# Performance work log

Measured on AMD Instinct MI355X. Metric: run time of the kernel, lower is better.

The kernel has to match this reference:

```python
import jax, jax.numpy as jnp
import numpy as np

B, L1, L2, H = 8, 384, 384, 128


def _lin(k, out_f, in_f, scale=0.05):
    kw, kb = jax.random.split(k)
    return (jax.random.normal(kw, (out_f, in_f), jnp.float32) * scale,
            jax.random.normal(kb, (out_f,), jnp.float32) * scale)


def setup_inputs() -> dict:
    key = jax.random.key(0)
    ks = jax.random.split(key, 10)
    Wq_w, Wq_b = _lin(ks[2], H, H)
    Wup_w, Wup_b = _lin(ks[3], H, H)
    Wvp_w, Wvp_b = _lin(ks[4], H, H)
    V_w, V_b = _lin(ks[5], 1, H)
    Wg_w, Wg_b = _lin(ks[6], 2 * H, 2 * H)
    W_ih, b_ih = _lin(ks[7], 4 * H, 2 * H)
    W_hh, b_hh = _lin(ks[8], 4 * H, H)
    return {
        "x": jax.random.normal(ks[0], (B, L1, H), jnp.float32),
        "x_mask": jnp.zeros((B, L1), dtype=bool),
        "y": jax.random.normal(ks[1], (B, L2, H), jnp.float32),
        "y_mask": jnp.zeros((B, L2), dtype=bool),
        "Wq_w": Wq_w, "Wq_b": Wq_b,
        "Wup_w": Wup_w, "Wup_b": Wup_b,
        "Wvp_w": Wvp_w, "Wvp_b": Wvp_b,
        "V_w": V_w, "V_b": V_b,
        "Wg_w": Wg_w, "Wg_b": Wg_b,
        "W_ih": W_ih, "W_hh": W_hh, "b_ih": b_ih, "b_hh": b_hh,
    }


def reference(x, x_mask, y, y_mask, Wq_w, Wq_b, Wup_w, Wup_b, Wvp_w, Wvp_b,
              V_w, V_b, Wg_w, Wg_b, W_ih, W_hh, b_ih, b_hh):
    b, l1, h = x.shape
    # projections (torch Linear: x @ W.T + b)
    x_proj = x @ Wup_w.T + Wup_b                      # [B, L1, H]
    y_proj = y @ Wq_w.T + Wq_b                        # [B, L2, H]
    # source feeds a constant zero hidden state into W_vp -> just its bias
    hidden_proj = jnp.zeros((h,), x.dtype) @ Wvp_w.T + Wvp_b  # [H]
    # additive attention scores: V . tanh(xp + yp + hp)
    sum_batch = jnp.tanh(x_proj[:, :, None, :] + y_proj[:, None, :, :] + hidden_proj)  # [B,L1,L2,H]
    s = jnp.einsum('btjh,h->btj', sum_batch, V_w[0]) + V_b[0]  # [B, L1, L2]
    # sum_mask = (1 - x_mask) outer (1 - y_mask)
    xm = 1.0 - x_mask.astype(s.dtype)
    ym = 1.0 - y_mask.astype(s.dtype)
    s = s * (xm[:, :, None] * ym[:, None, :])
    s = jnp.where(y_mask[:, None, :], -jnp.inf, s)
    alpha = jax.nn.softmax(s, axis=-1)                # [B, L1, L2]
    ct = jnp.einsum('btj,bjh->bth', alpha, y)         # [B, L1, H]
    merge = jnp.concatenate([x, ct], axis=2)          # [B, L1, 2H]
    gt = jax.nn.sigmoid(merge @ Wg_w.T + Wg_b)
    lstm_in = gt * merge                              # [B, L1, 2H]
    # single-layer unidirectional LSTM (torch gate order: i, f, g, o)
    gates_x = lstm_in @ W_ih.T + b_ih                 # [B, L1, 4H]

    def step(carry, gx):
        h_t, c_t = carry
        g = gx + h_t @ W_hh.T + b_hh
        i, f, gg, o = jnp.split(g, 4, axis=-1)
        c_n = jax.nn.sigmoid(f) * c_t + jax.nn.sigmoid(i) * jnp.tanh(gg)
        h_n = jax.nn.sigmoid(o) * jnp.tanh(c_n)
        return (h_n, c_n), h_n

    init = (jnp.zeros((b, h), x.dtype), jnp.zeros((b, h), x.dtype))
    _, hs = jax.lax.scan(step, init, jnp.swapaxes(gates_x, 0, 1))  # [L1, B, H]
    return jnp.swapaxes(hs, 0, 1)                     # [B, L1, H]
```

## Files before the change

kernel.cpp:

```cpp
#include <hip/hip_runtime.h>
#include <hip/hip_bf16.h>
#include <math.h>

typedef __attribute__((ext_vector_type(4))) float  float4v;
typedef __attribute__((ext_vector_type(2))) float  float2v;
typedef __attribute__((ext_vector_type(8))) short  short8;

#define B_ 8
#define L_ 384
#define H_ 128

__device__ __forceinline__ float bflo(unsigned int u){ unsigned int t = u << 16; float f; __builtin_memcpy(&f,&t,4); return f; }
__device__ __forceinline__ unsigned short f2bf(float f){
  unsigned int t; __builtin_memcpy(&t,&f,4);
  return (unsigned short)((t + 0x7fffu + ((t>>16)&1u)) >> 16);
}
__device__ __forceinline__ float fsig(float x){ return __fdividef(1.f, 1.f + __expf(-x)); }

__device__ __forceinline__ void barrier_lds(){
  asm volatile("s_waitcnt lgkmcnt(0)\n\ts_barrier" ::: "memory");
}

template<int K>
__device__ __forceinline__ void mfma_rowgemm_body(
    unsigned short* in_s,
    const float* __restrict__ inA, const float* __restrict__ inB,
    const float* __restrict__ W, const float* __restrict__ bias,
    const float* __restrict__ bias2, float* __restrict__ out,
    int Ntotal, int act, int row0, int ob)
{
  constexpr int KP = K + 2;
  const int tid  = threadIdx.x;
  const int w    = tid >> 6;
  const int l    = tid & 63;
  const int c    = l & 15;
  const int quad = l >> 4;

  #pragma unroll
  for (int it = 0; it < K/32; ++it) {
    int idx = it*256 + tid;
    int r = idx / (K/4);
    int k = (idx % (K/4)) * 4;
    float4v f;
    if (inB != nullptr && k >= 128)
      f = *(const float4v*)(inB + (size_t)(row0+r)*128 + (k-128));
    else if (inB != nullptr)
      f = *(const float4v*)(inA + (size_t)(row0+r)*128 + k);
    else
      f = *(const float4v*)(inA + (size_t)(row0+r)*K + k);
    unsigned int p0 = (unsigned int)f2bf(f.x) | ((unsigned int)f2bf(f.y) << 16);
    unsigned int p1 = (unsigned int)f2bf(f.z) | ((unsigned int)f2bf(f.w) << 16);
    *(unsigned int*)&in_s[r*KP + k]     = p0;
    *(unsigned int*)&in_s[r*KP + k + 2] = p1;
  }

  const int n = ob + w*16 + c;
  short8 bfr[K/32];
  #pragma unroll
  for (int kt = 0; kt < K/32; ++kt) {
    const float* src = W + (size_t)n*K + kt*32 + quad*8;
    float4v f0 = *(const float4v*)(src);
    float4v f1 = *(const float4v*)(src + 4);
    short8 v;
    v[0]=(short)f2bf(f0[0]); v[1]=(short)f2bf(f0[1]); v[2]=(short)f2bf(f0[2]); v[3]=(short)f2bf(f0[3]);
    v[4]=(short)f2bf(f1[0]); v[5]=(short)f2bf(f1[1]); v[6]=(short)f2bf(f1[2]); v[7]=(short)f2bf(f1[3]);
    bfr[kt] = v;
  }
  __syncthreads();

  const float4v z4 = {0.f,0.f,0.f,0.f};
  float4v acc0 = z4, acc1 = z4;
  #pragma unroll
  for (int kt = 0; kt < K/32; ++kt) {
    short8 a0 = *(const short8*)&in_s[(c     )*KP + kt*32 + quad*8];
    short8 a1 = *(const short8*)&in_s[(16 + c)*KP + kt*32 + quad*8];
    acc0 = __builtin_amdgcn_mfma_f32_16x16x32_bf16(a0, bfr[kt], acc0, 0,0,0);
    acc1 = __builtin_amdgcn_mfma_f32_16x16x32_bf16(a1, bfr[kt], acc1, 0,0,0);
  }

  float bv = bias[n] + (bias2 ? bias2[n] : 0.f);
  #pragma unroll
  for (int mt = 0; mt < 2; ++mt) {
    float4v A = mt ? acc1 : acc0;
    #pragma unroll
    for (int r = 0; r < 4; ++r) {
      int m = mt*16 + quad*4 + r;
      float val = A[r] + bv;
      if (act == 2) {
        float mg = bflo((unsigned int)in_s[m*KP + n]);
        val = fsig(val) * mg;
      }
      if (act == 3)
        out[(size_t)(row0+m)*Ntotal + (n & 127)*4 + (n >> 7)] = val;
      else
        out[(size_t)(row0+m)*Ntotal + n] = val;
    }
  }
}

template<int K>
__global__ __launch_bounds__(256) void mfma_rowgemm_kernel(
    const float* __restrict__ inA, const float* __restrict__ inB,
    const float* __restrict__ W, const float* __restrict__ bias,
    const float* __restrict__ bias2, float* __restrict__ out,
    int Ntotal, int act)
{
  __shared__ __align__(16) unsigned short in_s[32*(K+2)];
  mfma_rowgemm_body<K>(in_s, inA, inB, W, bias, bias2, out,
                       Ntotal, act, blockIdx.x*32, blockIdx.y*64);
}

__global__ __launch_bounds__(256) void proj_mfma_kernel(
    const float* __restrict__ x, const float* __restrict__ y,
    const float* __restrict__ Wup_w, const float* __restrict__ Wup_b,
    const float* __restrict__ Wq_w, const float* __restrict__ Wq_b,
    const float* __restrict__ Wvp_b,
    float* __restrict__ xp, float* __restrict__ yp)
{
  __shared__ __align__(16) unsigned short in_s[32*130];
  int bx = blockIdx.x;
  if (bx < 192)
    mfma_rowgemm_body<128>(in_s, x, nullptr, Wup_w, Wup_b, nullptr,
                           xp, 128, 0, (bx>>1)*32, (bx&1)*64);
  else {
    bx -= 192;
    mfma_rowgemm_body<128>(in_s, y, nullptr, Wq_w, Wq_b, Wvp_b,
                           yp, 128, 0, (bx>>1)*32, (bx&1)*64);
  }
}

__global__ __launch_bounds__(256) void attn_kernel(
    const float* __restrict__ xp, const float* __restrict__ yp,
    const float* __restrict__ y, const unsigned char* __restrict__ xmask,
    const unsigned char* __restrict__ ymask, const float* __restrict__ Vw,
    const float* __restrict__ Vb,
    float* __restrict__ ctp0, float* __restrict__ ctp1,
    float* __restrict__ ml)
{
  __shared__ __align__(16) float xp_s[8][128];
  __shared__ __align__(16) float v2_s[128];
  __shared__ __align__(16) float yp_s[32][132];
  __shared__ __align__(16) float yc_s[32][132];
  __shared__ float xm_s[8];
  __shared__ float ym_s[32];
  __shared__ float sv_s;
  const int tid = threadIdx.x;
  const int b   = blockIdx.y;
  const int t0  = blockIdx.x * 8;
  const int jh  = blockIdx.z;
  const float C2 = 2.8853900817779268f;
  {
    int r = tid >> 5, k4 = (tid & 31) * 4;
    float4v f = *(const float4v*)(xp + ((size_t)(b*L_ + t0 + r))*H_ + k4);
    float4v g; g[0]=f[0]*C2; g[1]=f[1]*C2; g[2]=f[2]*C2; g[3]=f[3]*C2;
    *(float4v*)&xp_s[r][k4] = g;
    if (tid < 32) {
      float4v v = *(const float4v*)(Vw + tid*4);
      float4v v2; v2[0]=2.f*v[0]; v2[1]=2.f*v[1]; v2[2]=2.f*v[2]; v2[3]=2.f*v[3];
      *(float4v*)&v2_s[tid*4] = v2;
    }
    if (tid < 8) xm_s[tid] = xmask[b*L_ + t0 + tid] ? 0.f : 1.f;
  }
  __syncthreads();
  if (tid < 32) {
    float4v v = *(const float4v*)&v2_s[tid*4];
    float sm = (v[0]+v[1]) + (v[2]+v[3]);
    #pragma unroll
    for (int off = 16; off >= 1; off >>= 1) sm += __shfl_xor(sm, off);
    if (tid == 0) sv_s = 0.5f*sm + Vb[0];
  }

  float4v rp[4], ry[4];
  unsigned char ymb = 0;
  {
    #pragma unroll
    for (int it = 0; it < 4; ++it) {
      int idx = it*256 + tid; int r = idx >> 5; int k4 = (idx & 31) * 4;
      size_t base = ((size_t)(b*L_ + jh*192 + r))*H_ + k4;
      rp[it] = *(const float4v*)(yp + base);
      ry[it] = *(const float4v*)(y + base);
    }
    if (tid < 32) ymb = ymask[b*L_ + jh*192 + tid];
  }

  const int t = tid >> 5, u = tid & 31;
  float mrun = -__builtin_inff(), lrun = 0.f;
  float a0=0.f, a1=0.f, a2=0.f, a3=0.f;
  float svc = 0.f, xmv = 0.f;

  for (int c = 0; c < 6; ++c) {
    __syncthreads();
    #pragma unroll
    for (int it = 0; it < 4; ++it) {
      int idx = it*256 + tid; int r = idx >> 5; int k4 = (idx & 31) * 4;
      float4v sp; sp[0]=rp[it][0]*C2; sp[1]=rp[it][1]*C2; sp[2]=rp[it][2]*C2; sp[3]=rp[it][3]*C2;
      *(float4v*)&yp_s[r][k4] = sp;
      *(float4v*)&yc_s[r][k4] = ry[it];
    }
    if (tid < 32) ym_s[tid] = ymb ? 0.f : 1.f;
    __syncthreads();
    if (c == 0) { svc = sv_s; xmv = xm_s[t]; }
    if (c < 5) {
      #pragma unroll
      for (int it = 0; it < 4; ++it) {
        int idx = it*256 + tid; int r = idx >> 5; int k4 = (idx & 31) * 4;
        size_t base = ((size_t)(b*L_ + jh*192 + (c+1)*32 + r))*H_ + k4;
        rp[it] = *(const float4v*)(yp + base);
        ry[it] = *(const float4v*)(y + base);
      }
      if (tid < 32) ymb = ymask[b*L_ + jh*192 + (c+1)*32 + tid];
    }

    float sA = 0.f, sB = 0.f;
    {
      const float* yr = yp_s[u];
      const float* xr = xp_s[t];
      #pragma unroll 4
      for (int k = 0; k < 128; k += 4) {
        float4v yv = *(const float4v*)&yr[k];
        float4v xv = *(const float4v*)&xr[k];
        float4v vv = *(const float4v*)&v2_s[k];
        float e0 = __builtin_amdgcn_exp2f(xv[0] + yv[0]);
        sA -= vv[0] * __builtin_amdgcn_rcpf(e0 + 1.f);
        float e1 = __builtin_amdgcn_exp2f(xv[1] + yv[1]);
        sB -= vv[1] * __builtin_amdgcn_rcpf(e1 + 1.f);
        float e2 = __builtin_amdgcn_exp2f(xv[2] + yv[2]);
        sA -= vv[2] * __builtin_amdgcn_rcpf(e2 + 1.f);
        float e3 = __builtin_amdgcn_exp2f(xv[3] + yv[3]);
        sB -= vv[3] * __builtin_amdgcn_rcpf(e3 + 1.f);
      }
    }
    float ymv = ym_s[u];
    float s = (svc + sA + sB) * xmv * ymv;
    if (ymv == 0.f) s = -__builtin_inff();
    float mc = s;
    #pragma unroll
    for (int off = 16; off >= 1; off >>= 1) mc = fmaxf(mc, __shfl_xor(mc, off));
    float mnew = fmaxf(mrun, mc);
    float p  = __expf(s - mnew);
    float sc = __expf(mrun - mnew);
    float ps = p;
    #pragma unroll
    for (int off = 16; off >= 1; off >>= 1) ps += __shfl_xor(ps, off);
    lrun = lrun * sc + ps;
    mrun = mnew;
    a0 *= sc; a1 *= sc; a2 *= sc; a3 *= sc;
    #pragma unroll 8
    for (int j = 0; j < 32; ++j) {
      float pv = __shfl(p, j, 32);
      float4v yv = *(const float4v*)&yc_s[j][u*4];
      a0 += pv*yv[0]; a1 += pv*yv[1]; a2 += pv*yv[2]; a3 += pv*yv[3];
    }
  }
  const int row = b*L_ + t0 + t;
  float* ctp = jh ? ctp1 : ctp0;
  float4v ov; ov[0]=a0; ov[1]=a1; ov[2]=a2; ov[3]=a3;
  *(float4v*)(ctp + (size_t)row*H_ + u*4) = ov;
  if (u == 0) {
    ml[(jh*2+0)*3072 + row] = mrun;
    ml[(jh*2+1)*3072 + row] = lrun;
  }
}

__global__ __launch_bounds__(256) void attn_merge_kernel(
    const float* __restrict__ ctp0, const float* __restrict__ ctp1,
    const float* __restrict__ ml, float* __restrict__ ct)
{
  const int tid = threadIdx.x;
  const int row = blockIdx.x*8 + (tid >> 5);
  const int c4  = (tid & 31) * 4;
  float m0 = ml[row],        l0 = ml[3072 + row];
  float m1 = ml[2*3072+row], l1 = ml[3*3072 + row];
  float m  = fmaxf(m0, m1);
  float e0 = __expf(m0 - m), e1 = __expf(m1 - m);
  float inv = __fdividef(1.f, l0*e0 + l1*e1);
  float4v v0 = *(const float4v*)(ctp0 + (size_t)row*H_ + c4);
  float4v v1 = *(const float4v*)(ctp1 + (size_t)row*H_ + c4);
  float4v r;
  r[0] = (v0[0]*e0 + v1[0]*e1)*inv;
  r[1] = (v0[1]*e0 + v1[1]*e1)*inv;
  r[2] = (v0[2]*e0 + v1[2]*e1)*inv;
  r[3] = (v0[3]*e0 + v1[3]*e1)*inv;
  *(float4v*)(ct + (size_t)row*H_ + c4) = r;
}

__global__ __launch_bounds__(512) void lstm_kernel(
    const float* __restrict__ gx, const float* __restrict__ Whh,
    float* __restrict__ out)
{
  __shared__ __align__(16) unsigned short h_s[2][128];
  const int tid  = threadIdx.x;
  const int b    = blockIdx.x;
  const int w    = tid >> 6;
  const int l    = tid & 63;
  const int col  = l & 15;
  const int quad = l >> 4;

  short8 bf[4][4];
  #pragma unroll
  for (int nt = 0; nt < 4; ++nt) {
    const int n = nt*128 + w*16 + col;
    #pragma unroll
    for (int kt = 0; kt < 4; ++kt) {
      const int k0 = kt*32 + quad*8;
      const float* src = Whh + (size_t)n*H_ + k0;
      float4v f0 = *(const float4v*)(src);
      float4v f1 = *(const float4v*)(src + 4);
      short8 v;
      v[0]=(short)f2bf(f0[0]); v[1]=(short)f2bf(f0[1]); v[2]=(short)f2bf(f0[2]); v[3]=(short)f2bf(f0[3]);
      v[4]=(short)f2bf(f1[0]); v[5]=(short)f2bf(f1[1]); v[6]=(short)f2bf(f1[2]); v[7]=(short)f2bf(f1[3]);
      bf[nt][kt] = v;
    }
  }

  if (tid < 128) { h_s[0][tid] = 0; h_s[1][tid] = 0; }
  float cst = 0.f;
  const int goff = w*16 + col;
  const float* gbase = gx + (size_t)b*L_*512 + goff*4;
  float* outp = out + (size_t)b*L_*H_ + goff;
  float4v gbuf[4];
  #pragma unroll
  for (int s = 0; s < 4; ++s)
    gbuf[s] = *(const float4v*)(gbase + (size_t)s*512);
  const float4v z4 = {0.f,0.f,0.f,0.f};
  const float NL2E = -1.4426950408889634f;
  const float P2L2E = 2.8853900817779268f;
  __syncthreads();

  for (int t4 = 0; t4 < L_; t4 += 4) {
    #pragma unroll
    for (int s = 0; s < 4; ++s) {
      const int tstep = t4 + s;
      const unsigned short* hb = h_s[s & 1];
      short8 a[4];
      #pragma unroll
      for (int kt=0;kt<4;++kt) a[kt] = *(const short8*)&hb[kt*32 + quad*8];
      float4v c0 = z4, c1 = z4, c2 = z4, c3 = z4;
      #pragma unroll
      for (int kt=0;kt<4;++kt) {
        c0 = __builtin_amdgcn_mfma_f32_16x16x32_bf16(a[kt], bf[0][kt], c0, 0,0,0);
        c1 = __builtin_amdgcn_mfma_f32_16x16x32_bf16(a[kt], bf[1][kt], c1, 0,0,0);
        c2 = __builtin_amdgcn_mfma_f32_16x16x32_bf16(a[kt], bf[2][kt], c2, 0,0,0);
        c3 = __builtin_amdgcn_mfma_f32_16x16x32_bf16(a[kt], bf[3][kt], c3, 0,0,0);
      }
      float g0 = c0[0] + gbuf[s][0];
      float g1 = c1[0] + gbuf[s][1];
      float g2 = c2[0] + gbuf[s][2];
      float g3 = c3[0] + gbuf[s][3];
      if (tstep + 4 < L_)
        gbuf[s] = *(const float4v*)(gbase + (size_t)(tstep+4)*512);
      if (quad == 0) {
        float ig = __builtin_amdgcn_rcpf(1.f + __builtin_amdgcn_exp2f(NL2E*g0));
        float fg = __builtin_amdgcn_rcpf(1.f + __builtin_amdgcn_exp2f(NL2E*g1));
        float gg = 1.f - 2.f*__builtin_amdgcn_rcpf(__builtin_amdgcn_exp2f(P2L2E*g2) + 1.f);
        float og = __builtin_amdgcn_rcpf(1.f + __builtin_amdgcn_exp2f(NL2E*g3));
        cst = fg*cst + ig*gg;
        float hn = og * (1.f - 2.f*__builtin_amdgcn_rcpf(__builtin_amdgcn_exp2f(P2L2E*cst) + 1.f));
        outp[(size_t)tstep*H_] = hn;
        h_s[(s+1)&1][goff] = f2bf(hn);
      }
      barrier_lds();
    }
  }
}

extern "C" void kernel_launch(void* const* d_in, const int* in_sizes, int n_in,
                              void* d_out, int out_size, void* d_ws, size_t ws_size,
                              hipStream_t stream)
{
  (void)in_sizes; (void)n_in; (void)out_size; (void)ws_size;
  const float* x     = (const float*)d_in[0];
  const unsigned char* xm = (const unsigned char*)d_in[1];
  const float* y     = (const float*)d_in[2];
  const unsigned char* ym = (const unsigned char*)d_in[3];
  const float* Wq_w  = (const float*)d_in[4];
  const float* Wq_b  = (const float*)d_in[5];
  const float* Wup_w = (const float*)d_in[6];
  const float* Wup_b = (const float*)d_in[7];
  const float* Wvp_b = (const float*)d_in[9];
  const float* V_w   = (const float*)d_in[10];
  const float* V_b   = (const float*)d_in[11];
  const float* Wg_w  = (const float*)d_in[12];
  const float* Wg_b  = (const float*)d_in[13];
  const float* W_ih  = (const float*)d_in[14];
  const float* W_hh  = (const float*)d_in[15];
  const float* b_ih  = (const float*)d_in[16];
  const float* b_hh  = (const float*)d_in[17];
  float* out = (float*)d_out;

  float* wsf    = (float*)d_ws;
  float* xp_ws  = wsf;
  float* yp_ws  = xp_ws + 393216;
  float* ct_ws  = yp_ws + 393216;
  float* li_ws  = ct_ws + 393216;
  float* gx_ws  = li_ws + 786432;
  float* ct2_ws = gx_ws + 1572864;
  float* ml_ws  = ct2_ws + 393216;

  proj_mfma_kernel<<<dim3(384),256,0,stream>>>(x, y, Wup_w, Wup_b, Wq_w, Wq_b, Wvp_b, xp_ws, yp_ws);
  attn_kernel<<<dim3(48,8,2),256,0,stream>>>(xp_ws, yp_ws, y, xm, ym, V_w, V_b, ct_ws, ct2_ws, ml_ws);
  attn_merge_kernel<<<dim3(384),256,0,stream>>>(ct_ws, ct2_ws, ml_ws, ct_ws);
  mfma_rowgemm_kernel<256><<<dim3(96,4),256,0,stream>>>(x, ct_ws, Wg_w, Wg_b, nullptr, li_ws, 256, 2);
  mfma_rowgemm_kernel<256><<<dim3(96,8),256,0,stream>>>(li_ws, nullptr, W_ih, b_ih, b_hh, gx_ws, 512, 3);
  lstm_kernel<<<dim3(8),512,0,stream>>>(gx_ws, W_hh, out);
}
```

Baseline: 345.4 us.

## Fuse attention merge, gate GEMM and input-gate GEMM into one kernel

Replaces the attention-merge kernel and the two row-GEMM launches (gate sigmoid and W_ih projection) with a single 48-block kernel. Each block merges the split-softmax partials on load, computes the gated LSTM input in LDS as bf16, then runs the W_ih GEMM straight from LDS. This removes two launches and the global round-trips for ct and lstm_in. In exchange there are only 48 blocks, so occupancy is low on a large GPU, and each block re-converts the full weight matrices.

```diff
diff --git a/kernel.cpp b/kernel.cpp
--- a/kernel.cpp
+++ b/kernel.cpp
@@ -24,10 +24,10 @@
 template<int K>
 __device__ __forceinline__ void mfma_rowgemm_body(
     unsigned short* in_s,
-    const float* __restrict__ inA, const float* __restrict__ inB,
+    const float* __restrict__ inA,
     const float* __restrict__ W, const float* __restrict__ bias,
     const float* __restrict__ bias2, float* __restrict__ out,
-    int Ntotal, int act, int row0, int ob)
+    int Ntotal, int row0, int ob)
 {
   constexpr int KP = K + 2;
   const int tid  = threadIdx.x;
@@ -41,13 +41,7 @@
     int idx = it*256 + tid;
     int r = idx / (K/4);
     int k = (idx % (K/4)) * 4;
-    float4v f;
-    if (inB != nullptr && k >= 128)
-      f = *(const float4v*)(inB + (size_t)(row0+r)*128 + (k-128));
-    else if (inB != nullptr)
-      f = *(const float4v*)(inA + (size_t)(row0+r)*128 + k);
-    else
-      f = *(const float4v*)(inA + (size_t)(row0+r)*K + k);
+    float4v f = *(const float4v*)(inA + (size_t)(row0+r)*K + k);
     unsigned int p0 = (unsigned int)f2bf(f.x) | ((unsigned int)f2bf(f.y) << 16);
     unsigned int p1 = (unsigned int)f2bf(f.z) | ((unsigned int)f2bf(f.w) << 16);
     *(unsigned int*)&in_s[r*KP + k]     = p0;
@@ -85,29 +79,9 @@
     #pragma unroll
     for (int r = 0; r < 4; ++r) {
       int m = mt*16 + quad*4 + r;
-      float val = A[r] + bv;
-      if (act == 2) {
-        float mg = bflo((unsigned int)in_s[m*KP + n]);
-        val = fsig(val) * mg;
-      }
-      if (act == 3)
-        out[(size_t)(row0+m)*Ntotal + (n & 127)*4 + (n >> 7)] = val;
-      else
-        out[(size_t)(row0+m)*Ntotal + n] = val;
-    }
-  }
-}
-
-template<int K>
-__global__ __launch_bounds__(256) void mfma_rowgemm_kernel(
-    const float* __restrict__ inA, const float* __restrict__ inB,
-    const float* __restrict__ W, const float* __restrict__ bias,
-    const float* __restrict__ bias2, float* __restrict__ out,
-    int Ntotal, int act)
-{
-  __shared__ __align__(16) unsigned short in_s[32*(K+2)];
-  mfma_rowgemm_body<K>(in_s, inA, inB, W, bias, bias2, out,
-                       Ntotal, act, blockIdx.x*32, blockIdx.y*64);
+      out[(size_t)(row0+m)*Ntotal + n] = A[r] + bv;
+    }
+  }
 }
 
 __global__ __launch_bounds__(256) void proj_mfma_kernel(
@@ -120,12 +94,12 @@
   __shared__ __align__(16) unsigned short in_s[32*130];
   int bx = blockIdx.x;
   if (bx < 192)
-    mfma_rowgemm_body<128>(in_s, x, nullptr, Wup_w, Wup_b, nullptr,
-                           xp, 128, 0, (bx>>1)*32, (bx&1)*64);
+    mfma_rowgemm_body<128>(in_s, x, Wup_w, Wup_b, nullptr,
+                           xp, 128, (bx>>1)*32, (bx&1)*64);
   else {
     bx -= 192;
-    mfma_rowgemm_body<128>(in_s, y, nullptr, Wq_w, Wq_b, Wvp_b,
-                           yp, 128, 0, (bx>>1)*32, (bx&1)*64);
+    mfma_rowgemm_body<128>(in_s, y, Wq_w, Wq_b, Wvp_b,
+                           yp, 128, (bx>>1)*32, (bx&1)*64);
   }
 }
 
@@ -262,26 +236,152 @@
   }
 }
 
-__global__ __launch_bounds__(256) void attn_merge_kernel(
+__global__ __launch_bounds__(512) void fused_gate_kernel(
+    const float* __restrict__ x,
     const float* __restrict__ ctp0, const float* __restrict__ ctp1,
-    const float* __restrict__ ml, float* __restrict__ ct)
+    const float* __restrict__ ml,
+    const float* __restrict__ Wg_w, const float* __restrict__ Wg_b,
+    const float* __restrict__ W_ih, const float* __restrict__ b_ih,
+    const float* __restrict__ b_hh, float* __restrict__ gx)
 {
-  const int tid = threadIdx.x;
-  const int row = blockIdx.x*8 + (tid >> 5);
-  const int c4  = (tid & 31) * 4;
-  float m0 = ml[row],        l0 = ml[3072 + row];
-  float m1 = ml[2*3072+row], l1 = ml[3*3072 + row];
-  float m  = fmaxf(m0, m1);
-  float e0 = __expf(m0 - m), e1 = __expf(m1 - m);
-  float inv = __fdividef(1.f, l0*e0 + l1*e1);
-  float4v v0 = *(const float4v*)(ctp0 + (size_t)row*H_ + c4);
-  float4v v1 = *(const float4v*)(ctp1 + (size_t)row*H_ + c4);
-  float4v r;
-  r[0] = (v0[0]*e0 + v1[0]*e1)*inv;
-  r[1] = (v0[1]*e0 + v1[1]*e1)*inv;
-  r[2] = (v0[2]*e0 + v1[2]*e1)*inv;
-  r[3] = (v0[3]*e0 + v1[3]*e1)*inv;
-  *(float4v*)(ct + (size_t)row*H_ + c4) = r;
+  constexpr int KP = 258;
+  constexpr int LP = 264;
+  __shared__ __align__(16) unsigned short in_s[64*KP];
+  __shared__ __align__(16) unsigned short li_s[64*LP];
+  const int tid  = threadIdx.x;
+  const int w    = tid >> 6;
+  const int l    = tid & 63;
+  const int c    = l & 15;
+  const int quad = l >> 4;
+  const int row0 = blockIdx.x * 64;
+  const float4v z4 = {0.f,0.f,0.f,0.f};
+
+  #pragma unroll
+  for (int it = 0; it < 8; ++it) {
+    int idx = it*512 + tid;
+    int r = idx >> 6;
+    int k = (idx & 63) * 4;
+    int row = row0 + r;
+    float4v f;
+    if (k < 128) {
+      f = *(const float4v*)(x + (size_t)row*128 + k);
+    } else {
+      float m0 = ml[row],        l0 = ml[3072 + row];
+      float m1 = ml[2*3072+row], l1 = ml[3*3072 + row];
+      float mm = fmaxf(m0, m1);
+      float e0 = __expf(m0 - mm), e1 = __expf(m1 - mm);
+      float inv = __fdividef(1.f, l0*e0 + l1*e1);
+      float4v v0 = *(const float4v*)(ctp0 + (size_t)row*128 + (k-128));
+      float4v v1 = *(const float4v*)(ctp1 + (size_t)row*128 + (k-128));
+      f[0] = (v0[0]*e0 + v1[0]*e1)*inv;
+      f[1] = (v0[1]*e0 + v1[1]*e1)*inv;
+      f[2] = (v0[2]*e0 + v1[2]*e1)*inv;
+      f[3] = (v0[3]*e0 + v1[3]*e1)*inv;
+    }
+    unsigned int p0 = (unsigned int)f2bf(f[0]) | ((unsigned int)f2bf(f[1]) << 16);
+    unsigned int p1 = (unsigned int)f2bf(f[2]) | ((unsigned int)f2bf(f[3]) << 16);
+    *(unsigned int*)&in_s[r*KP + k]     = p0;
+    *(unsigned int*)&in_s[r*KP + k + 2] = p1;
+  }
+  __syncthreads();
+
+  {
+    short8 bfr[2][8];
+    #pragma unroll
+    for (int i = 0; i < 2; ++i) {
+      int n = (w + i*8)*16 + c;
+      #pragma unroll
+      for (int kt = 0; kt < 8; ++kt) {
+        const float* src = Wg_w + (size_t)n*256 + kt*32 + quad*8;
+        float4v f0 = *(const float4v*)(src);
+        float4v f1 = *(const float4v*)(src + 4);
+        short8 v;
+        v[0]=(short)f2bf(f0[0]); v[1]=(short)f2bf(f0[1]); v[2]=(short)f2bf(f0[2]); v[3]=(short)f2bf(f0[3]);
+        v[4]=(short)f2bf(f1[0]); v[5]=(short)f2bf(f1[1]); v[6]=(short)f2bf(f1[2]); v[7]=(short)f2bf(f1[3]);
+        bfr[i][kt] = v;
+      }
+    }
+    float4v acc[2][4];
+    #pragma unroll
+    for (int i=0;i<2;++i)
+      #pragma unroll
+      for (int mt=0;mt<4;++mt) acc[i][mt] = z4;
+    #pragma unroll
+    for (int kt = 0; kt < 8; ++kt) {
+      short8 a[4];
+      #pragma unroll
+      for (int mt = 0; mt < 4; ++mt)
+        a[mt] = *(const short8*)&in_s[(mt*16 + c)*KP + kt*32 + quad*8];
+      #pragma unroll
+      for (int i = 0; i < 2; ++i)
+        #pragma unroll
+        for (int mt = 0; mt < 4; ++mt)
+          acc[i][mt] = __builtin_amdgcn_mfma_f32_16x16x32_bf16(a[mt], bfr[i][kt], acc[i][mt], 0,0,0);
+    }
+    #pragma unroll
+    for (int i = 0; i < 2; ++i) {
+      int n = (w + i*8)*16 + c;
+      float bv = Wg_b[n];
+      #pragma unroll
+      for (int mt = 0; mt < 4; ++mt)
+        #pragma unroll
+        for (int r = 0; r < 4; ++r) {
+          int m = mt*16 + quad*4 + r;
+          float val = acc[i][mt][r] + bv;
+          float mg = bflo((unsigned int)in_s[m*KP + n]);
+          li_s[m*LP + n] = f2bf(fsig(val) * mg);
+        }
+    }
+  }
+  __syncthreads();
+
+  #pragma unroll
+  for (int p = 0; p < 2; ++p) {
+    short8 bfr[2][8];
+    #pragma unroll
+    for (int i = 0; i < 2; ++i) {
+      int n = (w + i*8 + p*16)*16 + c;
+      #pragma unroll
+      for (int kt = 0; kt < 8; ++kt) {
+        const float* src = W_ih + (size_t)n*256 + kt*32 + quad*8;
+        float4v f0 = *(const float4v*)(src);
+        float4v f1 = *(const float4v*)(src + 4);
+        short8 v;
+        v[0]=(short)f2bf(f0[0]); v[1]=(short)f2bf(f0[1]); v[2]=(short)f2bf(f0[2]); v[3]=(short)f2bf(f0[3]);
+        v[4]=(short)f2bf(f1[0]); v[5]=(short)f2bf(f1[1]); v[6]=(short)f2bf(f1[2]); v[7]=(short)f2bf(f1[3]);
+        bfr[i][kt] = v;
+      }
+    }
+    float4v acc[2][4];
+    #pragma unroll
+    for (int i=0;i<2;++i)
+      #pragma unroll
+      for (int mt=0;mt<4;++mt) acc[i][mt] = z4;
+    #pragma unroll
+    for (int kt = 0; kt < 8; ++kt) {
+      short8 a[4];
+      #pragma unroll
+      for (int mt = 0; mt < 4; ++mt)
+        a[mt] = *(const short8*)&li_s[(mt*16 + c)*LP + kt*32 + quad*8];
+      #pragma unroll
+      for (int i = 0; i < 2; ++i)
+        #pragma unroll
+        for (int mt = 0; mt < 4; ++mt)
+          acc[i][mt] = __builtin_amdgcn_mfma_f32_16x16x32_bf16(a[mt], bfr[i][kt], acc[i][mt], 0,0,0);
+    }
+    #pragma unroll
+    for (int i = 0; i < 2; ++i) {
+      int n = (w + i*8 + p*16)*16 + c;
+      float bv = b_ih[n] + b_hh[n];
+      #pragma unroll
+      for (int mt = 0; mt < 4; ++mt)
+        #pragma unroll
+        for (int r = 0; r < 4; ++r) {
+          int m = mt*16 + quad*4 + r;
+          gx[(size_t)(row0+m)*512 + (n & 127)*4 + (n >> 7)] = acc[i][mt][r] + bv;
+        }
+    }
+  }
 }
 
 __global__ __launch_bounds__(512) void lstm_kernel(
@@ -391,16 +491,14 @@
   float* wsf    = (float*)d_ws;
   float* xp_ws  = wsf;
   float* yp_ws  = xp_ws + 393216;
-  float* ct_ws  = yp_ws + 393216;
-  float* li_ws  = ct_ws + 393216;
-  float* gx_ws  = li_ws + 786432;
-  float* ct2_ws = gx_ws + 1572864;
-  float* ml_ws  = ct2_ws + 393216;
+  float* ctp0_ws= yp_ws + 393216;
+  float* ctp1_ws= ctp0_ws + 393216;
+  float* gx_ws  = ctp1_ws + 393216;
+  float* ml_ws  = gx_ws + 1572864;
 
   proj_mfma_kernel<<<dim3(384),256,0,stream>>>(x, y, Wup_w, Wup_b, Wq_w, Wq_b, Wvp_b, xp_ws, yp_ws);
-  attn_kernel<<<dim3(48,8,2),256,0,stream>>>(xp_ws, yp_ws, y, xm, ym, V_w, V_b, ct_ws, ct2_ws, ml_ws);
-  attn_merge_kernel<<<dim3(384),256,0,stream>>>(ct_ws, ct2_ws, ml_ws, ct_ws);
-  mfma_rowgemm_kernel<256><<<dim3(96,4),256,0,stream>>>(x, ct_ws, Wg_w, Wg_b, nullptr, li_ws, 256, 2);
-  mfma_rowgemm_kernel<256><<<dim3(96,8),256,0,stream>>>(li_ws, nullptr, W_ih, b_ih, b_hh, gx_ws, 512, 3);
+  attn_kernel<<<dim3(48,8,2),256,0,stream>>>(xp_ws, yp_ws, y, xm, ym, V_w, V_b, ctp0_ws, ctp1_ws, ml_ws);
+  fused_gate_kernel<<<dim3(48),512,0,stream>>>(x, ctp0_ws, ctp1_ws, ml_ws,
+                                               Wg_w, Wg_b, W_ih, b_ih, b_hh, gx_ws);
   lstm_kernel<<<dim3(8),512,0,stream>>>(gx_ws, W_hh, out);
 }
```

After: 359.4 us. 1.04x slower.
